# Kernel optimization log

Measured on AMD Instinct MI355X. Metric: run time of the kernel, lower is better.

## Reference

```python
import jax, jax.numpy as jnp
import numpy as np

B, N, DIM = 8, 2048, 1024
E, HID = 8, 2048
EPS = 1e-9
THRESHOLD = 0.2          # second_threshold_eval
CAP_FACTOR = 2.0         # capacity_factor_eval
MIN_EXPERT_CAPACITY = 4
LOSS_COEF = 0.01
CAPACITY = max(min(N, int(N * CAP_FACTOR / E)), MIN_EXPERT_CAPACITY)  # 512


def setup_inputs() -> dict:
    key = jax.random.key(0)
    k = jax.random.split(key, 5)
    x = jax.random.normal(k[0], (B, N, DIM), jnp.float32)
    # gating weight: nn.Parameter(torch.randn(dim, num_gates))
    w_gating = jax.random.normal(k[1], (DIM, E), jnp.float32)
    # expert weights: init_ -> uniform(-1/sqrt(last_dim), 1/sqrt(last_dim))
    s1 = 1.0 / np.sqrt(HID)
    s2 = 1.0 / np.sqrt(DIM)
    w1 = jax.random.uniform(k[2], (E, DIM, HID), jnp.float32, -s1, s1)
    w2 = jax.random.uniform(k[3], (E, HID, DIM), jnp.float32, -s2, s2)
    # uniform noise for the 'random' second-expert policy (torch: .uniform_(0,1))
    rand_probs = jax.random.uniform(k[4], (B, N), jnp.float32)
    return {"x": x, "w_gating": w_gating, "w1": w1, "w2": w2, "rand_probs": rand_probs}


def _cumsum_exclusive(t):
    # exclusive cumsum along token axis (-2)
    return jnp.cumsum(t, axis=-2) - t


def _safe_one_hot(idx, maxlen):
    # indices may equal maxlen (overflow slot) -> dropped column
    return jax.nn.one_hot(idx, maxlen + 1, dtype=jnp.float32)[..., :maxlen]


def reference(x, w_gating, w1, w2, rand_probs):
    b, n, d = x.shape
    e, cap = E, CAPACITY
    capf = float(cap)

    # ---- Top2Gating ----
    raw_gates = jax.nn.softmax(jnp.einsum('bnd,de->bne', x, w_gating), axis=-1)
    gate_1 = jnp.max(raw_gates, axis=-1)
    index_1 = jnp.argmax(raw_gates, axis=-1)
    mask_1 = jax.nn.one_hot(index_1, e, dtype=jnp.float32)        # [b,n,e]
    density_1_proxy = raw_gates

    gates_wo_1 = raw_gates * (1.0 - mask_1)
    gate_2 = jnp.max(gates_wo_1, axis=-1)
    index_2 = jnp.argmax(gates_wo_1, axis=-1)
    mask_2 = jax.nn.one_hot(index_2, e, dtype=jnp.float32)

    denom = gate_1 + gate_2 + EPS
    gate_1 = gate_1 / denom
    gate_2 = gate_2 / denom

    # load-balance loss
    density_1 = jnp.mean(mask_1, axis=-2)                          # [b,e]
    loss = jnp.mean(jnp.mean(density_1_proxy, axis=-2) * density_1) * float(e ** 2)

    # second policy: 'random' -> keep 2nd expert with prob proportional to gate_2
    keep_2 = (rand_probs < (gate_2 / max(THRESHOLD, EPS))).astype(jnp.float32)
    mask_2 = mask_2 * keep_2[..., None]

    # positions within expert capacity
    position_in_expert_1 = _cumsum_exclusive(mask_1) * mask_1
    mask_1 = mask_1 * (position_in_expert_1 < capf).astype(jnp.float32)
    mask_1_count = jnp.sum(mask_1, axis=-2, keepdims=True)         # [b,1,e]
    mask_1_flat = jnp.sum(mask_1, axis=-1)                          # [b,n]
    position_in_expert_1 = jnp.sum(position_in_expert_1, axis=-1)   # [b,n]
    gate_1 = gate_1 * mask_1_flat

    position_in_expert_2 = (_cumsum_exclusive(mask_2) + mask_1_count) * mask_2
    mask_2 = mask_2 * (position_in_expert_2 < capf).astype(jnp.float32)
    mask_2_flat = jnp.sum(mask_2, axis=-1)
    position_in_expert_2 = jnp.sum(position_in_expert_2, axis=-1)
    gate_2 = gate_2 * mask_2_flat

    # combine tensor [b, n, e, cap]
    combine_tensor = (
        gate_1[..., None, None] * mask_1_flat[..., None, None]
        * jax.nn.one_hot(index_1, e, dtype=jnp.float32)[..., None]
        * _safe_one_hot(position_in_expert_1.astype(jnp.int32), cap)[..., None, :]
        + gate_2[..., None, None] * mask_2_flat[..., None, None]
        * jax.nn.one_hot(index_2, e, dtype=jnp.float32)[..., None]
        * _safe_one_hot(position_in_expert_2.astype(jnp.int32), cap)[..., None, :]
    )
    dispatch_tensor = (combine_tensor != 0.0).astype(combine_tensor.dtype)

    # ---- dispatch -> expert FFN -> combine ----
    expert_inputs = jnp.einsum('bnd,bnec->ebcd', x, dispatch_tensor)  # [e,b,cap,d]
    ei = expert_inputs.reshape(e, -1, d)                              # [e, b*cap, d]
    hidden = jax.nn.gelu(jnp.einsum('etd,edh->eth', ei, w1), approximate=False)
    expert_out = jnp.einsum('eth,ehd->etd', hidden, w2).reshape(e, b, cap, d)
    output = jnp.einsum('ebcd,bnec->bnd', expert_out, combine_tensor)
    return output, loss * LOSS_COEF
```

## Files before the change

### kernel.cpp

```cpp
#include <hip/hip_runtime.h>
#include <hip/hip_bf16.h>

typedef unsigned short u16;
typedef unsigned int u32;

typedef short short8 __attribute__((ext_vector_type(8)));
typedef float f32x4 __attribute__((ext_vector_type(4)));

constexpr int Bc   = 8;
constexpr int Nc   = 2048;
constexpr int DIMc = 1024;
constexpr int Ec   = 8;
constexpr int HIDc = 2048;
constexpr int CAPc = 512;
constexpr int NTOK   = Bc * Nc;
constexpr int SLOTPE = Bc * CAPc;
constexpr int NSLOT  = Ec * SLOTPE;

constexpr size_t OFF_SLOTTOK = 0;
constexpr size_t OFF_SGATE   = OFF_SLOTTOK + (size_t)NSLOT * 4;
constexpr size_t OFF_G1      = OFF_SGATE + (size_t)NSLOT * 4;
constexpr size_t OFF_G2      = OFF_G1 + (size_t)NTOK * 4;
constexpr size_t OFF_META    = OFF_G2 + (size_t)NTOK * 4;
constexpr size_t OFF_S1      = OFF_META + (size_t)NTOK * 4;
constexpr size_t OFF_S2      = OFF_S1 + (size_t)NTOK * 4;
constexpr size_t OFF_RAW     = OFF_S2 + (size_t)NTOK * 4;
constexpr size_t OFF_S       = OFF_RAW + (size_t)NTOK * 8 * 4;
constexpr size_t OFF_C       = OFF_S + 64 * 4;
constexpr size_t MISC_SZ     = 2 << 20;
static_assert(OFF_C + 64 * 4 <= MISC_SZ, "misc overflow");

constexpr size_t SZ_W1T_E = (size_t)HIDc * DIMc * 2;
constexpr size_t SZ_W2T_E = (size_t)DIMc * HIDc * 2;
constexpr size_t SZ_EI_E  = (size_t)SLOTPE * DIMc * 2;
constexpr size_t SZ_HID_E = (size_t)SLOTPE * HIDc * 2;
constexpr size_t SZ_EO    = (size_t)NSLOT * DIMc * 2;

__device__ __host__ inline size_t layout_need(int epr) {
    return SZ_EO + (size_t)epr * (SZ_W1T_E + SZ_W2T_E + SZ_EI_E + SZ_HID_E) + MISC_SZ;
}

__device__ inline u16 f2bf(float f) {
    u32 u = __float_as_uint(f);
    u32 r = (u + 0x7fffu + ((u >> 16) & 1u)) >> 16;
    return (u16)r;
}
__device__ inline u32 pack2(float lo, float hi) {
    return (u32)f2bf(lo) | ((u32)f2bf(hi) << 16);
}
__device__ inline float bflo(u32 u) { return __uint_as_float(u << 16); }
__device__ inline float bfhi(u32 u) { return __uint_as_float(u & 0xffff0000u); }

__device__ inline float gelu_fast(float v) {
    const float u = v * (0.7978845608028654f + 0.0356774081363001f * v * v);
    return v / (1.f + __builtin_exp2f(-2.885390081777927f * u));
}

#define GLDS16(gp, lp)                                                          \
    __builtin_amdgcn_global_load_lds(                                          \
        (const __attribute__((address_space(1))) void*)(gp),                   \
        (__attribute__((address_space(3))) void*)(lp), 16, 0, 0)

__global__ __launch_bounds__(256) void init_slots_kernel(int* __restrict__ slot_token) {
    int i = (blockIdx.x * 256 + threadIdx.x) * 4;
    slot_token[i] = -1; slot_token[i + 1] = -1; slot_token[i + 2] = -1; slot_token[i + 3] = -1;
}

__global__ __launch_bounds__(256) void gate_kernel(
    const float* __restrict__ x, const float* __restrict__ wg,
    const float* __restrict__ rp, float* __restrict__ raw_out,
    float* __restrict__ g1_out, float* __restrict__ g2_out, int* __restrict__ meta_out)
{
    const int tk   = blockIdx.x * 4 + (threadIdx.x >> 6);
    const int lane = threadIdx.x & 63;
    const float* xr = x + (size_t)tk * DIMc;

    float acc[8] = {0.f, 0.f, 0.f, 0.f, 0.f, 0.f, 0.f, 0.f};
#pragma unroll
    for (int i = 0; i < 4; ++i) {
        const int d0 = i * 256 + lane * 4;
        float4 xv = *(const float4*)(xr + d0);
#pragma unroll
        for (int j = 0; j < 4; ++j) {
            float xs = (&xv.x)[j];
            float4 w0 = *(const float4*)(wg + (size_t)(d0 + j) * 8);
            float4 w1 = *(const float4*)(wg + (size_t)(d0 + j) * 8 + 4);
            acc[0] += xs * w0.x; acc[1] += xs * w0.y; acc[2] += xs * w0.z; acc[3] += xs * w0.w;
            acc[4] += xs * w1.x; acc[5] += xs * w1.y; acc[6] += xs * w1.z; acc[7] += xs * w1.w;
        }
    }
#pragma unroll
    for (int e = 0; e < 8; ++e) {
#pragma unroll
        for (int off = 1; off < 64; off <<= 1) acc[e] += __shfl_xor(acc[e], off);
    }

    if (lane == 0) {
        float mx = acc[0];
#pragma unroll
        for (int e = 1; e < 8; ++e) mx = fmaxf(mx, acc[e]);
        float ex[8], s = 0.f;
#pragma unroll
        for (int e = 0; e < 8; ++e) { ex[e] = expf(acc[e] - mx); s += ex[e]; }
        float inv = 1.f / s;
        float raw[8];
#pragma unroll
        for (int e = 0; e < 8; ++e) raw[e] = ex[e] * inv;

        int i1 = 0; float g1 = raw[0];
#pragma unroll
        for (int e = 1; e < 8; ++e) if (raw[e] > g1) { g1 = raw[e]; i1 = e; }
        int i2 = -1; float g2 = -1.f;
#pragma unroll
        for (int e = 0; e < 8; ++e) if (e != i1 && raw[e] > g2) { g2 = raw[e]; i2 = e; }

        float denom = g1 + g2 + 1e-9f;
        float g1n = g1 / denom, g2n = g2 / denom;
        int keep = (rp[tk] < (g2n / 0.2f)) ? 1 : 0;

        float* ro = raw_out + (size_t)tk * 8;
#pragma unroll
        for (int e = 0; e < 8; ++e) ro[e] = raw[e];
        g1_out[tk] = g1n;
        g2_out[tk] = g2n;
        meta_out[tk] = i1 | (i2 << 4) | (keep << 8);
    }
}

__global__ __launch_bounds__(256) void scan_kernel(
    const int* __restrict__ meta, const float* __restrict__ g1, const float* __restrict__ g2,
    int* __restrict__ slot_token, int* __restrict__ slot1, int* __restrict__ slot2)
{
    const int b = blockIdx.x;
    const int t = threadIdx.x;
    __shared__ int cnt[256][8];
    __shared__ int base_e[8];

    int m[8];
#pragma unroll
    for (int i = 0; i < 8; ++i) m[i] = meta[b * Nc + t * 8 + i];

    int c[8] = {0, 0, 0, 0, 0, 0, 0, 0};
#pragma unroll
    for (int i = 0; i < 8; ++i) c[m[i] & 15]++;
#pragma unroll
    for (int e = 0; e < 8; ++e) cnt[t][e] = c[e];
    __syncthreads();
    if (t < 8) {
        int run = 0;
        for (int i = 0; i < 256; ++i) { int v = cnt[i][t]; cnt[i][t] = run; run += v; }
        base_e[t] = run < CAPc ? run : CAPc;
    }
    __syncthreads();
#pragma unroll
    for (int e = 0; e < 8; ++e) c[e] = cnt[t][e];
#pragma unroll
    for (int i = 0; i < 8; ++i) {
        const int tk = b * Nc + t * 8 + i;
        const int e = m[i] & 15;
        const int pos = c[e]++;
        if (pos < CAPc) {
            const int slot = ((e * Bc + b) << 9) | pos;
            slot_token[slot] = tk;
            slot1[tk] = slot;
        } else {
            slot1[tk] = -1;
        }
    }
    __syncthreads();

#pragma unroll
    for (int e = 0; e < 8; ++e) c[e] = 0;
#pragma unroll
    for (int i = 0; i < 8; ++i) {
        if ((m[i] >> 8) & 1) c[(m[i] >> 4) & 15]++;
    }
#pragma unroll
    for (int e = 0; e < 8; ++e) cnt[t][e] = c[e];
    __syncthreads();
    if (t < 8) {
        int run = 0;
        for (int i = 0; i < 256; ++i) { int v = cnt[i][t]; cnt[i][t] = run; run += v; }
    }
    __syncthreads();
#pragma unroll
    for (int e = 0; e < 8; ++e) c[e] = cnt[t][e];
#pragma unroll
    for (int i = 0; i < 8; ++i) {
        const int tk = b * Nc + t * 8 + i;
        int s2v = -1;
        if ((m[i] >> 8) & 1) {
            const int e = (m[i] >> 4) & 15;
            const int pos = base_e[e] + c[e]++;
            if (pos < CAPc) {
                const int slot = ((e * Bc + b) << 9) | pos;
                slot_token[slot] = tk;
                s2v = slot;
            }
        }
        slot2[tk] = s2v;
    }
}

__global__ __launch_bounds__(256) void reduce_stats_kernel(
    const float* __restrict__ raw, const int* __restrict__ meta,
    float* __restrict__ S, float* __restrict__ C)
{
    const int be = blockIdx.x, b = be >> 3, e = be & 7;
    float s = 0.f, c = 0.f;
    for (int n = threadIdx.x; n < Nc; n += 256) {
        const int tk = b * Nc + n;
        s += raw[(size_t)tk * 8 + e];
        c += ((meta[tk] & 15) == e) ? 1.f : 0.f;
    }
    __shared__ float sh_s[4], sh_c[4];
    const int lane = threadIdx.x & 63, wv = threadIdx.x >> 6;
#pragma unroll
    for (int off = 32; off; off >>= 1) { s += __shfl_down(s, off); c += __shfl_down(c, off); }
    if (lane == 0) { sh_s[wv] = s; sh_c[wv] = c; }
    __syncthreads();
    if (threadIdx.x == 0) {
        S[be] = sh_s[0] + sh_s[1] + sh_s[2] + sh_s[3];
        C[be] = sh_c[0] + sh_c[1] + sh_c[2] + sh_c[3];
    }
}

__global__ void loss_kernel(const float* __restrict__ S, const float* __restrict__ C,
                            float* __restrict__ dst)
{
    float v = S[threadIdx.x] * C[threadIdx.x];
#pragma unroll
    for (int off = 32; off; off >>= 1) v += __shfl_down(v, off);
    if (threadIdx.x == 0) *dst = v * (0.01f / ((float)Nc * (float)Nc));
}

template <int R, int C>
__global__ __launch_bounds__(256) void transpose_kernel(
    const float* __restrict__ w, u16* __restrict__ wT, const int e0)
{
    __shared__ float tile[32][33];
    const int ez = blockIdx.z;
    const int c0 = blockIdx.x * 32, r0 = blockIdx.y * 32;
    const float* src = w + (size_t)(e0 + ez) * R * C;
    u16* dst = wT + (size_t)ez * C * R;
    const int t = threadIdx.x;
#pragma unroll
    for (int i = 0; i < 4; ++i) {
        const int r = i * 8 + (t >> 5), cc = t & 31;
        tile[r][cc] = src[(size_t)(r0 + r) * C + c0 + cc];
    }
    __syncthreads();
#pragma unroll
    for (int i = 0; i < 4; ++i) {
        const int cc = i * 8 + (t >> 5), r = t & 31;
        dst[(size_t)(c0 + cc) * R + r0 + r] = f2bf(tile[r][cc]);
    }
}

__global__ __launch_bounds__(256) void gather_kernel(
    const float* __restrict__ x, const int* __restrict__ slot_token,
    u16* __restrict__ ei, const int slot0)
{
    const int s = blockIdx.x * 4 + (threadIdx.x >> 6);
    const int lane = threadIdx.x & 63;
    const int tk = slot_token[slot0 + s];
    uint4* dst = (uint4*)(ei + ((size_t)s << 10)) + lane * 2;
    if (tk < 0) {
        uint4 z = {0u, 0u, 0u, 0u};
        dst[0] = z; dst[1] = z;
    } else {
        const float4* src = (const float4*)(x + ((size_t)tk << 10)) + lane * 4;
        float4 v0 = src[0], v1 = src[1], v2 = src[2], v3 = src[3];
        uint4 o0, o1;
        o0.x = pack2(v0.x, v0.y); o0.y = pack2(v0.z, v0.w);
        o0.z = pack2(v1.x, v1.y); o0.w = pack2(v1.z, v1.w);
        o1.x = pack2(v2.x, v2.y); o1.y = pack2(v2.z, v2.w);
        o1.z = pack2(v3.x, v3.y); o1.w = pack2(v3.z, v3.w);
        dst[0] = o0; dst[1] = o1;
    }
}


template <int K, bool GELU>
__device__ inline void gemm_body(
    const u16* __restrict__ A, const u16* __restrict__ Bt, u16* __restrict__ Cc,
    const int nB, const int ldc)
{
    __shared__ u16 As[128 * 64];
    __shared__ u16 Bs[128 * 64];

    const int tid = threadIdx.x;
    const int wv = tid >> 6, lane = tid & 63;

    const int MT = gridDim.x;
    const int lin = blockIdx.y * MT + blockIdx.x;
    const int nb  = MT * gridDim.y;
    const int per = nb >> 3;
    const int sid = (lin & 7) * per + (lin >> 3);
    const int gsz = MT << 2;
    const int g   = sid / gsz;
    const int r   = sid - g * gsz;
    const int mt  = r >> 2;
    const int nt  = (g << 2) + (r & 3);

    const int m0 = mt * 128, n0 = nt * 128;
    const int e = mt >> 5;

    const int wr = wv >> 1, wc = wv & 1;
    const int lr = lane & 15, lk = lane >> 4;

    const int rb = tid >> 3;
    const int gc = (((tid & 7) ^ ((tid >> 3) & 7)) * 8);

    const u16* pa0 = A + (size_t)(m0 + rb) * K + gc;
    const u16* pa1 = pa0 + (size_t)32 * K;
    const u16* pa2 = pa0 + (size_t)64 * K;
    const u16* pa3 = pa0 + (size_t)96 * K;
    const u16* pbb = Bt + ((size_t)e * nB + n0 + rb) * K + gc;
    const u16* pb1 = pbb + (size_t)32 * K;
    const u16* pb2 = pbb + (size_t)64 * K;
    const u16* pb3 = pbb + (size_t)96 * K;

    u16* la = As + tid * 8;
    u16* lb = Bs + tid * 8;

    f32x4 acc[4][4];
#pragma unroll
    for (int i = 0; i < 4; ++i)
#pragma unroll
        for (int j = 0; j < 4; ++j) acc[i][j] = (f32x4)0.f;

    for (int k0 = 0; k0 < K; k0 += 64) {
        __syncthreads();
        GLDS16(pa0, la);        GLDS16(pa1, la + 2048);
        GLDS16(pa2, la + 4096); GLDS16(pa3, la + 6144);
        GLDS16(pbb, lb);        GLDS16(pb1, lb + 2048);
        GLDS16(pb2, lb + 4096); GLDS16(pb3, lb + 6144);
        pa0 += 64; pa1 += 64; pa2 += 64; pa3 += 64;
        pbb += 64; pb1 += 64; pb2 += 64; pb3 += 64;
        __syncthreads();

#pragma unroll
        for (int kk = 0; kk < 2; ++kk) {
            const int sl = ((kk * 4 + lk) ^ (lr & 7)) * 8;
            short8 a[4], b[4];
#pragma unroll
            for (int f = 0; f < 4; ++f) {
                a[f] = *(const short8*)(As + (wr * 64 + f * 16 + lr) * 64 + sl);
                b[f] = *(const short8*)(Bs + (wc * 64 + f * 16 + lr) * 64 + sl);
            }
#pragma unroll
            for (int fm = 0; fm < 4; ++fm)
#pragma unroll
                for (int fn = 0; fn < 4; ++fn)
                    acc[fm][fn] = __builtin_amdgcn_mfma_f32_16x16x32_bf16(
                        a[fm], b[fn], acc[fm][fn], 0, 0, 0);
        }
    }

#pragma unroll
    for (int fm = 0; fm < 4; ++fm) {
        const int row = m0 + wr * 64 + fm * 16 + lk * 4;
#pragma unroll
        for (int fn = 0; fn < 4; ++fn) {
            const int col = n0 + wc * 64 + fn * 16 + lr;
#pragma unroll
            for (int r2 = 0; r2 < 4; ++r2) {
                float v = acc[fm][fn][r2];
                if (GELU) v = gelu_fast(v);
                Cc[(size_t)(row + r2) * ldc + col] = f2bf(v);
            }
        }
    }
}

__global__ __launch_bounds__(256, 4) void gemm1_kernel(
    const u16* __restrict__ A, const u16* __restrict__ Bt, u16* __restrict__ Cc)
{
    gemm_body<DIMc, true>(A, Bt, Cc, HIDc, HIDc);
}

__global__ __launch_bounds__(256, 4) void gemm2_kernel(
    const u16* __restrict__ A, const u16* __restrict__ Bt, u16* __restrict__ Cc)
{
    gemm_body<HIDc, false>(A, Bt, Cc, DIMc, DIMc);
}

__global__ __launch_bounds__(256) void combine_kernel(
    const u16* __restrict__ eo, const int* __restrict__ slot1, const int* __restrict__ slot2,
    const float* __restrict__ g1, const float* __restrict__ g2, float* __restrict__ out)
{
    const int tk = blockIdx.x * 4 + (threadIdx.x >> 6);
    const int lane = threadIdx.x & 63;
    int s1 = slot1[tk], s2 = slot2[tk];
    const float a = (s1 >= 0) ? g1[tk] : 0.f;
    const float b = (s2 >= 0) ? g2[tk] : 0.f;
    if (s1 < 0) s1 = 0;
    if (s2 < 0) s2 = 0;
    const uint4* p1 = (const uint4*)(eo + ((size_t)s1 << 10)) + lane * 2;
    const uint4* p2 = (const uint4*)(eo + ((size_t)s2 << 10)) + lane * 2;
    uint4 x0 = p1[0], x1 = p1[1];
    uint4 y0 = p2[0], y1 = p2[1];
    float4* dst = (float4*)(out + ((size_t)tk << 10)) + lane * 4;
    float4 o;
    o.x = a * bflo(x0.x) + b * bflo(y0.x); o.y = a * bfhi(x0.x) + b * bfhi(y0.x);
    o.z = a * bflo(x0.y) + b * bflo(y0.y); o.w = a * bfhi(x0.y) + b * bfhi(y0.y);
    dst[0] = o;
    o.x = a * bflo(x0.z) + b * bflo(y0.z); o.y = a * bfhi(x0.z) + b * bfhi(y0.z);
    o.z = a * bflo(x0.w) + b * bflo(y0.w); o.w = a * bfhi(x0.w) + b * bfhi(y0.w);
    dst[1] = o;
    o.x = a * bflo(x1.x) + b * bflo(y1.x); o.y = a * bfhi(x1.x) + b * bfhi(y1.x);
    o.z = a * bflo(x1.y) + b * bflo(y1.y); o.w = a * bfhi(x1.y) + b * bfhi(y1.y);
    dst[2] = o;
    o.x = a * bflo(x1.z) + b * bflo(y1.z); o.y = a * bfhi(x1.z) + b * bfhi(y1.z);
    o.z = a * bflo(x1.w) + b * bflo(y1.w); o.w = a * bfhi(x1.w) + b * bfhi(y1.w);
    dst[3] = o;
}

extern "C" void kernel_launch(void* const* d_in, const int* in_sizes, int n_in,
                              void* d_out, int out_size, void* d_ws, size_t ws_size,
                              hipStream_t stream)
{
    (void)in_sizes; (void)n_in; (void)out_size;

    const float* x  = (const float*)d_in[0];
    const float* wg = (const float*)d_in[1];
    const float* w1 = (const float*)d_in[2];
    const float* w2 = (const float*)d_in[3];
    const float* rp = (const float*)d_in[4];
    float* out = (float*)d_out;
    char* ws = (char*)d_ws;

    int epr = 4;
    while (epr > 1 && layout_need(epr) > ws_size) epr >>= 1;
    if (layout_need(epr) > ws_size) return;

    u16* eo  = (u16*)(ws);
    u16* w1T = (u16*)(ws + SZ_EO);
    u16* w2T = (u16*)(ws + SZ_EO + (size_t)epr * SZ_W1T_E);
    u16* ei  = (u16*)(ws + SZ_EO + (size_t)epr * (SZ_W1T_E + SZ_W2T_E));
    u16* hid = (u16*)(ws + SZ_EO + (size_t)epr * (SZ_W1T_E + SZ_W2T_E + SZ_EI_E));
    char* misc = ws + SZ_EO + (size_t)epr * (SZ_W1T_E + SZ_W2T_E + SZ_EI_E + SZ_HID_E);

    int* slot_token = (int*)(misc + OFF_SLOTTOK);
    float* g1 = (float*)(misc + OFF_G1);
    float* g2 = (float*)(misc + OFF_G2);
    int* meta = (int*)(misc + OFF_META);
    int* s1 = (int*)(misc + OFF_S1);
    int* s2 = (int*)(misc + OFF_S2);
    float* raw = (float*)(misc + OFF_RAW);
    float* Sr = (float*)(misc + OFF_S);
    float* C1 = (float*)(misc + OFF_C);

    init_slots_kernel<<<NSLOT / 1024, 256, 0, stream>>>(slot_token);
    gate_kernel<<<NTOK / 4, 256, 0, stream>>>(x, wg, rp, raw, g1, g2, meta);
    scan_kernel<<<Bc, 256, 0, stream>>>(meta, g1, g2, slot_token, s1, s2);
    reduce_stats_kernel<<<64, 256, 0, stream>>>(raw, meta, Sr, C1);
    loss_kernel<<<1, 64, 0, stream>>>(Sr, C1, out + (size_t)NTOK * DIMc);

    for (int e0 = 0; e0 < Ec; e0 += epr) {
        transpose_kernel<DIMc, HIDc><<<dim3(HIDc / 32, DIMc / 32, epr), 256, 0, stream>>>(
            w1, w1T, e0);
        transpose_kernel<HIDc, DIMc><<<dim3(DIMc / 32, HIDc / 32, epr), 256, 0, stream>>>(
            w2, w2T, e0);
        gather_kernel<<<epr * SLOTPE / 4, 256, 0, stream>>>(x, slot_token, ei, e0 * SLOTPE);

        gemm1_kernel<<<dim3(epr * 32, HIDc / 128), 256, 0, stream>>>(ei, w1T, hid);
        gemm2_kernel<<<dim3(epr * 32, DIMc / 128), 256, 0, stream>>>(
            hid, w2T, eo + (size_t)e0 * SLOTPE * DIMc);
    }

    combine_kernel<<<NTOK / 4, 256, 0, stream>>>(eo, s1, s2, g1, g2, out);
}
```

Before: 459.1 us.

## Fuse token gather into gemm1 via indexed A loads from bf16 x copy

The gate kernel now also writes a bf16 copy of x. gemm1 loads A rows straight from that copy, using slot_token indices and a zero page for empty slots, so the separate gather kernel and the ei buffer are gone. Slot initialisation moves from its own kernel into scan_kernel. This removes two kernel launches and the write-then-read round trip of the expert input buffer. The cost is a full bf16 copy of x written up front and scattered row reads inside the GEMM.

```diff
diff --git a/kernel.cpp b/kernel.cpp
--- a/kernel.cpp
+++ b/kernel.cpp
@@ -18,8 +18,7 @@
 constexpr int NSLOT  = Ec * SLOTPE;
 
 constexpr size_t OFF_SLOTTOK = 0;
-constexpr size_t OFF_SGATE   = OFF_SLOTTOK + (size_t)NSLOT * 4;
-constexpr size_t OFF_G1      = OFF_SGATE + (size_t)NSLOT * 4;
+constexpr size_t OFF_G1      = OFF_SLOTTOK + (size_t)NSLOT * 4;
 constexpr size_t OFF_G2      = OFF_G1 + (size_t)NTOK * 4;
 constexpr size_t OFF_META    = OFF_G2 + (size_t)NTOK * 4;
 constexpr size_t OFF_S1      = OFF_META + (size_t)NTOK * 4;
@@ -27,17 +26,18 @@
 constexpr size_t OFF_RAW     = OFF_S2 + (size_t)NTOK * 4;
 constexpr size_t OFF_S       = OFF_RAW + (size_t)NTOK * 8 * 4;
 constexpr size_t OFF_C       = OFF_S + 64 * 4;
+constexpr size_t OFF_ZP      = OFF_C + 64 * 4;
 constexpr size_t MISC_SZ     = 2 << 20;
-static_assert(OFF_C + 64 * 4 <= MISC_SZ, "misc overflow");
+static_assert(OFF_ZP + 2048 <= MISC_SZ, "misc overflow");
 
 constexpr size_t SZ_W1T_E = (size_t)HIDc * DIMc * 2;
 constexpr size_t SZ_W2T_E = (size_t)DIMc * HIDc * 2;
-constexpr size_t SZ_EI_E  = (size_t)SLOTPE * DIMc * 2;
 constexpr size_t SZ_HID_E = (size_t)SLOTPE * HIDc * 2;
 constexpr size_t SZ_EO    = (size_t)NSLOT * DIMc * 2;
+constexpr size_t SZ_XBF   = (size_t)NTOK * DIMc * 2;
 
 __device__ __host__ inline size_t layout_need(int epr) {
-    return SZ_EO + (size_t)epr * (SZ_W1T_E + SZ_W2T_E + SZ_EI_E + SZ_HID_E) + MISC_SZ;
+    return SZ_EO + SZ_XBF + (size_t)epr * (SZ_W1T_E + SZ_W2T_E + SZ_HID_E) + MISC_SZ;
 }
 
 __device__ inline u16 f2bf(float f) {
@@ -61,25 +61,26 @@
         (const __attribute__((address_space(1))) void*)(gp),                   \
         (__attribute__((address_space(3))) void*)(lp), 16, 0, 0)
 
-__global__ __launch_bounds__(256) void init_slots_kernel(int* __restrict__ slot_token) {
-    int i = (blockIdx.x * 256 + threadIdx.x) * 4;
-    slot_token[i] = -1; slot_token[i + 1] = -1; slot_token[i + 2] = -1; slot_token[i + 3] = -1;
-}
-
 __global__ __launch_bounds__(256) void gate_kernel(
     const float* __restrict__ x, const float* __restrict__ wg,
     const float* __restrict__ rp, float* __restrict__ raw_out,
-    float* __restrict__ g1_out, float* __restrict__ g2_out, int* __restrict__ meta_out)
+    float* __restrict__ g1_out, float* __restrict__ g2_out, int* __restrict__ meta_out,
+    u16* __restrict__ xbf)
 {
     const int tk   = blockIdx.x * 4 + (threadIdx.x >> 6);
     const int lane = threadIdx.x & 63;
     const float* xr = x + (size_t)tk * DIMc;
+    u16* xb = xbf + (size_t)tk * DIMc;
 
     float acc[8] = {0.f, 0.f, 0.f, 0.f, 0.f, 0.f, 0.f, 0.f};
 #pragma unroll
     for (int i = 0; i < 4; ++i) {
         const int d0 = i * 256 + lane * 4;
         float4 xv = *(const float4*)(xr + d0);
+        uint2 pk;
+        pk.x = pack2(xv.x, xv.y);
+        pk.y = pack2(xv.z, xv.w);
+        *(uint2*)(xb + d0) = pk;
 #pragma unroll
         for (int j = 0; j < 4; ++j) {
             float xs = (&xv.x)[j];
@@ -129,12 +130,20 @@
 
 __global__ __launch_bounds__(256) void scan_kernel(
     const int* __restrict__ meta, const float* __restrict__ g1, const float* __restrict__ g2,
-    int* __restrict__ slot_token, int* __restrict__ slot1, int* __restrict__ slot2)
+    int* __restrict__ slot_token, int* __restrict__ slot1, int* __restrict__ slot2,
+    u32* __restrict__ zp)
 {
     const int b = blockIdx.x;
     const int t = threadIdx.x;
     __shared__ int cnt[256][8];
     __shared__ int base_e[8];
+
+#pragma unroll
+    for (int j = 0; j < 16; ++j) {
+        const int idx = t * 16 + j;
+        slot_token[(((idx >> 9) * Bc + b) << 9) | (idx & 511)] = -1;
+    }
+    if (b == 0) { zp[t * 2] = 0u; zp[t * 2 + 1] = 0u; }
 
     int m[8];
 #pragma unroll
@@ -257,41 +266,7 @@
     }
 }
 
-__global__ __launch_bounds__(256) void gather_kernel(
-    const float* __restrict__ x, const int* __restrict__ slot_token,
-    u16* __restrict__ ei, const int slot0)
-{
-    const int s = blockIdx.x * 4 + (threadIdx.x >> 6);
-    const int lane = threadIdx.x & 63;
-    const int tk = slot_token[slot0 + s];
-    uint4* dst = (uint4*)(ei + ((size_t)s << 10)) + lane * 2;
-    if (tk < 0) {
-        uint4 z = {0u, 0u, 0u, 0u};
-        dst[0] = z; dst[1] = z;
-    } else {
-        const float4* src = (const float4*)(x + ((size_t)tk << 10)) + lane * 4;
-        float4 v0 = src[0], v1 = src[1], v2 = src[2], v3 = src[3];
-        uint4 o0, o1;
-        o0.x = pack2(v0.x, v0.y); o0.y = pack2(v0.z, v0.w);
-        o0.z = pack2(v1.x, v1.y); o0.w = pack2(v1.z, v1.w);
-        o1.x = pack2(v2.x, v2.y); o1.y = pack2(v2.z, v2.w);
-        o1.z = pack2(v3.x, v3.y); o1.w = pack2(v3.z, v3.w);
-        dst[0] = o0; dst[1] = o1;
-    }
-}
-
-
-template <int K, bool GELU>
-__device__ inline void gemm_body(
-    const u16* __restrict__ A, const u16* __restrict__ Bt, u16* __restrict__ Cc,
-    const int nB, const int ldc)
-{
-    __shared__ u16 As[128 * 64];
-    __shared__ u16 Bs[128 * 64];
-
-    const int tid = threadIdx.x;
-    const int wv = tid >> 6, lane = tid & 63;
-
+__device__ inline void tile_swizzle(int& mt, int& nt) {
     const int MT = gridDim.x;
     const int lin = blockIdx.y * MT + blockIdx.x;
     const int nb  = MT * gridDim.y;
@@ -300,9 +275,107 @@
     const int gsz = MT << 2;
     const int g   = sid / gsz;
     const int r   = sid - g * gsz;
-    const int mt  = r >> 2;
-    const int nt  = (g << 2) + (r & 3);
-
+    mt = r >> 2;
+    nt = (g << 2) + (r & 3);
+}
+
+__global__ __launch_bounds__(256, 4) void gemm1_kernel(
+    const u16* __restrict__ xbf, const int* __restrict__ slot_tok_round,
+    const u16* __restrict__ Bt, u16* __restrict__ Cc, const u16* __restrict__ zp)
+{
+    constexpr int K = DIMc;
+    __shared__ u16 As[128 * 64];
+    __shared__ u16 Bs[128 * 64];
+
+    const int tid = threadIdx.x;
+    const int wv = tid >> 6, lane = tid & 63;
+
+    int mt, nt;
+    tile_swizzle(mt, nt);
+    const int m0 = mt * 128, n0 = nt * 128;
+    const int e = mt >> 5;
+
+    const int wr = wv >> 1, wc = wv & 1;
+    const int lr = lane & 15, lk = lane >> 4;
+
+    const int rb = tid >> 3;
+    const int gc = (((tid & 7) ^ ((tid >> 3) & 7)) * 8);
+
+    const u16* pa[4];
+#pragma unroll
+    for (int p = 0; p < 4; ++p) {
+        const int tk = slot_tok_round[m0 + rb + 32 * p];
+        pa[p] = ((tk >= 0) ? xbf + ((size_t)tk << 10) : zp) + gc;
+    }
+    const u16* pbb = Bt + ((size_t)e * HIDc + n0 + rb) * K + gc;
+    const u16* pb1 = pbb + (size_t)32 * K;
+    const u16* pb2 = pbb + (size_t)64 * K;
+    const u16* pb3 = pbb + (size_t)96 * K;
+
+    u16* la = As + tid * 8;
+    u16* lb = Bs + tid * 8;
+
+    f32x4 acc[4][4];
+#pragma unroll
+    for (int i = 0; i < 4; ++i)
+#pragma unroll
+        for (int j = 0; j < 4; ++j) acc[i][j] = (f32x4)0.f;
+
+    for (int k0 = 0; k0 < K; k0 += 64) {
+        __syncthreads();
+        GLDS16(pa[0], la);        GLDS16(pa[1], la + 2048);
+        GLDS16(pa[2], la + 4096); GLDS16(pa[3], la + 6144);
+        GLDS16(pbb, lb);          GLDS16(pb1, lb + 2048);
+        GLDS16(pb2, lb + 4096);   GLDS16(pb3, lb + 6144);
+#pragma unroll
+        for (int p = 0; p < 4; ++p) pa[p] += 64;
+        pbb += 64; pb1 += 64; pb2 += 64; pb3 += 64;
+        __syncthreads();
+
+#pragma unroll
+        for (int kk = 0; kk < 2; ++kk) {
+            const int sl = ((kk * 4 + lk) ^ (lr & 7)) * 8;
+            short8 a[4], b[4];
+#pragma unroll
+            for (int f = 0; f < 4; ++f) {
+                a[f] = *(const short8*)(As + (wr * 64 + f * 16 + lr) * 64 + sl);
+                b[f] = *(const short8*)(Bs + (wc * 64 + f * 16 + lr) * 64 + sl);
+            }
+#pragma unroll
+            for (int fm = 0; fm < 4; ++fm)
+#pragma unroll
+                for (int fn = 0; fn < 4; ++fn)
+                    acc[fm][fn] = __builtin_amdgcn_mfma_f32_16x16x32_bf16(
+                        a[fm], b[fn], acc[fm][fn], 0, 0, 0);
+        }
+    }
+
+#pragma unroll
+    for (int fm = 0; fm < 4; ++fm) {
+        const int row = m0 + wr * 64 + fm * 16 + lk * 4;
+#pragma unroll
+        for (int fn = 0; fn < 4; ++fn) {
+            const int col = n0 + wc * 64 + fn * 16 + lr;
+#pragma unroll
+            for (int r2 = 0; r2 < 4; ++r2) {
+                Cc[(size_t)(row + r2) * HIDc + col] = f2bf(gelu_fast(acc[fm][fn][r2]));
+            }
+        }
+    }
+}
+
+__global__ __launch_bounds__(256, 4) void gemm2_kernel(
+    const u16* __restrict__ A, const u16* __restrict__ Bt, u16* __restrict__ Cc)
+{
+    constexpr int K = HIDc;
+    __shared__ u16 As[128 * 64];
+    __shared__ u16 Bs[128 * 64];
+
+    const int tid = threadIdx.x;
+    const int wv = tid >> 6, lane = tid & 63;
+
+    int mt, nt;
+    tile_swizzle(mt, nt);
     const int m0 = mt * 128, n0 = nt * 128;
     const int e = mt >> 5;
 
@@ -316,7 +389,7 @@
     const u16* pa1 = pa0 + (size_t)32 * K;
     const u16* pa2 = pa0 + (size_t)64 * K;
     const u16* pa3 = pa0 + (size_t)96 * K;
-    const u16* pbb = Bt + ((size_t)e * nB + n0 + rb) * K + gc;
+    const u16* pbb = Bt + ((size_t)e * DIMc + n0 + rb) * K + gc;
     const u16* pb1 = pbb + (size_t)32 * K;
     const u16* pb2 = pbb + (size_t)64 * K;
     const u16* pb3 = pbb + (size_t)96 * K;
@@ -366,24 +439,10 @@
             const int col = n0 + wc * 64 + fn * 16 + lr;
 #pragma unroll
             for (int r2 = 0; r2 < 4; ++r2) {
-                float v = acc[fm][fn][r2];
-                if (GELU) v = gelu_fast(v);
-                Cc[(size_t)(row + r2) * ldc + col] = f2bf(v);
+                Cc[(size_t)(row + r2) * DIMc + col] = f2bf(acc[fm][fn][r2]);
             }
         }
     }
-}
-
-__global__ __launch_bounds__(256, 4) void gemm1_kernel(
-    const u16* __restrict__ A, const u16* __restrict__ Bt, u16* __restrict__ Cc)
-{
-    gemm_body<DIMc, true>(A, Bt, Cc, HIDc, HIDc);
-}
-
-__global__ __launch_bounds__(256, 4) void gemm2_kernel(
-    const u16* __restrict__ A, const u16* __restrict__ Bt, u16* __restrict__ Cc)
-{
-    gemm_body<HIDc, false>(A, Bt, Cc, DIMc, DIMc);
 }
 
 __global__ __launch_bounds__(256) void combine_kernel(
@@ -436,11 +495,11 @@
     if (layout_need(epr) > ws_size) return;
 
     u16* eo  = (u16*)(ws);
-    u16* w1T = (u16*)(ws + SZ_EO);
-    u16* w2T = (u16*)(ws + SZ_EO + (size_t)epr * SZ_W1T_E);
-    u16* ei  = (u16*)(ws + SZ_EO + (size_t)epr * (SZ_W1T_E + SZ_W2T_E));
-    u16* hid = (u16*)(ws + SZ_EO + (size_t)epr * (SZ_W1T_E + SZ_W2T_E + SZ_EI_E));
-    char* misc = ws + SZ_EO + (size_t)epr * (SZ_W1T_E + SZ_W2T_E + SZ_EI_E + SZ_HID_E);
+    u16* xbf = (u16*)(ws + SZ_EO);
+    u16* w1T = (u16*)(ws + SZ_EO + SZ_XBF);
+    u16* w2T = (u16*)(ws + SZ_EO + SZ_XBF + (size_t)epr * SZ_W1T_E);
+    u16* hid = (u16*)(ws + SZ_EO + SZ_XBF + (size_t)epr * (SZ_W1T_E + SZ_W2T_E));
+    char* misc = ws + SZ_EO + SZ_XBF + (size_t)epr * (SZ_W1T_E + SZ_W2T_E + SZ_HID_E);
 
     int* slot_token = (int*)(misc + OFF_SLOTTOK);
     float* g1 = (float*)(misc + OFF_G1);
@@ -451,10 +510,10 @@
     float* raw = (float*)(misc + OFF_RAW);
     float* Sr = (float*)(misc + OFF_S);
     float* C1 = (float*)(misc + OFF_C);
-
-    init_slots_kernel<<<NSLOT / 1024, 256, 0, stream>>>(slot_token);
-    gate_kernel<<<NTOK / 4, 256, 0, stream>>>(x, wg, rp, raw, g1, g2, meta);
-    scan_kernel<<<Bc, 256, 0, stream>>>(meta, g1, g2, slot_token, s1, s2);
+    u16* zp = (u16*)(misc + OFF_ZP);
+
+    gate_kernel<<<NTOK / 4, 256, 0, stream>>>(x, wg, rp, raw, g1, g2, meta, xbf);
+    scan_kernel<<<Bc, 256, 0, stream>>>(meta, g1, g2, slot_token, s1, s2, (u32*)zp);
     reduce_stats_kernel<<<64, 256, 0, stream>>>(raw, meta, Sr, C1);
     loss_kernel<<<1, 64, 0, stream>>>(Sr, C1, out + (size_t)NTOK * DIMc);
 
@@ -463,9 +522,9 @@
             w1, w1T, e0);
         transpose_kernel<HIDc, DIMc><<<dim3(DIMc / 32, HIDc / 32, epr), 256, 0, stream>>>(
             w2, w2T, e0);
-        gather_kernel<<<epr * SLOTPE / 4, 256, 0, stream>>>(x, slot_token, ei, e0 * SLOTPE);
-
-        gemm1_kernel<<<dim3(epr * 32, HIDc / 128), 256, 0, stream>>>(ei, w1T, hid);
+
+        gemm1_kernel<<<dim3(epr * 32, HIDc / 128), 256, 0, stream>>>(
+            xbf, slot_token + e0 * SLOTPE, w1T, hid, zp);
         gemm2_kernel<<<dim3(epr * 32, DIMc / 128), 256, 0, stream>>>(
             hid, w2T, eo + (size_t)e0 * SLOTPE * DIMc);
     }
```

Result: faster. 429.8 us (-6.4%).
